# Kernel optimization log

Hardware: AMD Instinct MI355X
Metric: run time of the kernel (lower is better)

## Reference

```python
import jax, jax.numpy as jnp
import numpy as np

B, N = 8, 4096
NPOINT, RADIUS, NSAMPLE = 1024, 0.5, 32
IN_C = 64
MLP = [64, 64, 128]
EPS = 1e-5


def _gather(p, idx):
    # p: (B,N,C), idx: (B,...) int -> (B,...,C)
    return jax.vmap(lambda a, i: a[i])(p, idx)


def farthest_point_sample(xyz, npoint):
    b, n, _ = xyz.shape
    def step(carry, _):
        distance, farthest = carry
        centroid = _gather(xyz, farthest[:, None])              # (B,1,3)
        d = jnp.sum((xyz - centroid) ** 2, axis=-1)             # (B,N)
        distance = jnp.minimum(distance, d)
        nxt = jnp.argmax(distance, axis=-1).astype(jnp.int32)
        return (distance, nxt), farthest
    init = (jnp.full((b, n), 1e10, xyz.dtype), jnp.zeros((b,), jnp.int32))
    _, idx = jax.lax.scan(step, init, None, length=npoint)
    return idx.T                                                 # (B,npoint)


def query_ball_point(radius, nsample, xyz, new_xyz):
    b, n, _ = xyz.shape
    s = new_xyz.shape[1]
    sqr = jnp.sum((new_xyz[:, :, None, :] - xyz[:, None, :, :]) ** 2, axis=-1)  # (B,S,N)
    grp = jnp.broadcast_to(jnp.arange(n, dtype=jnp.int32), (b, s, n))
    grp = jnp.where(sqr > radius ** 2, n, grp)
    grp = jnp.sort(grp, axis=-1)[:, :, :nsample]                 # (B,S,K)
    first = grp[:, :, :1]
    return jnp.where(grp == n, first, grp)


def _sa_forward(xyz, points, params):
    fps_idx = farthest_point_sample(xyz, NPOINT)
    new_xyz = _gather(xyz, fps_idx)                              # (B,S,3)
    idx = query_ball_point(RADIUS, NSAMPLE, xyz, new_xyz)        # (B,S,K)
    grouped_xyz = _gather(xyz, idx)                              # (B,S,K,3)
    grouped_norm = grouped_xyz - new_xyz[:, :, None, :]
    grouped_pts = _gather(points, idx)                           # (B,S,K,C)
    feat = jnp.concatenate([grouped_xyz, grouped_norm, grouped_pts], axis=-1)
    for w, bias, gamma, beta in params:
        feat = jnp.einsum('bski,oi->bsko', feat, w) + bias       # 1x1 conv
        mean = feat.mean(axis=(0, 1, 2))                         # BN (train stats)
        var = feat.var(axis=(0, 1, 2))
        feat = (feat - mean) * jax.lax.rsqrt(var + EPS) * gamma + beta
        feat = jax.nn.relu(feat)
    new_points = feat.max(axis=2)                                # max over neighbors
    return new_xyz, new_points


def setup_inputs() -> dict:
    key = jax.random.key(0)
    ks = jax.random.split(key, 8)
    inp = {
        'xyz': jax.random.normal(ks[0], (B, N, 3), jnp.float32),
        'points': jax.random.normal(ks[1], (B, N, IN_C), jnp.float32),
    }
    last = IN_C + 6
    for li, out in enumerate(MLP):
        inp[f'w{li}'] = jax.random.normal(ks[2 + li], (out, last), jnp.float32) * 0.05
        inp[f'b{li}'] = jnp.zeros((out,), jnp.float32)
        inp[f'g{li}'] = jnp.ones((out,), jnp.float32)
        inp[f'be{li}'] = jnp.zeros((out,), jnp.float32)
        last = out
    return inp


def reference(xyz, points, w0, b0, g0, be0, w1, b1, g1, be1, w2, b2, g2, be2):
    params = [(w0, b0, g0, be0), (w1, b1, g1, be1), (w2, b2, g2, be2)]
    return _sa_forward(xyz, points, params)
```

## Files before the change

kernel.cpp:

```cpp
#include <hip/hip_runtime.h>

#define DI __device__ __forceinline__

#define B_ 8
#define N_ 4096
#define S_ 1024
#define K_ 32
#define M_TOT (B_ * S_ * K_)
#define NBLK 2048
#define NW 4096

typedef short bf16x8 __attribute__((ext_vector_type(8)));
typedef float f32x4 __attribute__((ext_vector_type(4)));

DI float sqdist_rn(float ax, float ay, float az, float bx, float by, float bz) {
    float dx = __fsub_rn(ax, bx);
    float dy = __fsub_rn(ay, by);
    float dz = __fsub_rn(az, bz);
    return __fadd_rn(__fadd_rn(__fmul_rn(dx, dx), __fmul_rn(dy, dy)), __fmul_rn(dz, dz));
}

DI unsigned short f2b(float f) {
    unsigned u = __float_as_uint(f);
    return (unsigned short)((u + 0x7FFFu + ((u >> 16) & 1u)) >> 16);
}
DI float b2f(unsigned short h) { return __uint_as_float(((unsigned)h) << 16); }

template <int CTRL>
DI unsigned long long dpp_u64(unsigned long long v) {
    unsigned lo = (unsigned)__builtin_amdgcn_update_dpp(
        0, (int)(unsigned)v, CTRL, 0xF, 0xF, true);
    unsigned hi = (unsigned)__builtin_amdgcn_update_dpp(
        0, (int)(unsigned)(v >> 32), CTRL, 0xF, 0xF, true);
    return ((unsigned long long)hi << 32) | lo;
}
DI unsigned long long umax64(unsigned long long a, unsigned long long b) {
    return a > b ? a : b;
}

__global__ __launch_bounds__(512) void fps_kernel(const float* __restrict__ xyz,
                                                  float* __restrict__ new_xyz) {
    const int b = blockIdx.x;
    const int t = threadIdx.x;
    const float* X = xyz + (size_t)b * (N_ * 3);
    __shared__ float4 pts[N_];
    __shared__ __align__(16) unsigned long long part[2][8];
    float px[8], py[8], pz[8], dd[8];
#pragma unroll
    for (int j = 0; j < 8; ++j) {
        int p = t + 512 * j;
        float x = X[p * 3 + 0], y = X[p * 3 + 1], z = X[p * 3 + 2];
        px[j] = x; py[j] = y; pz[j] = z; dd[j] = 1e10f;
        pts[p] = make_float4(x, y, z, 0.0f);
    }
    if (t == 0) {
        new_xyz[(size_t)b * (S_ * 3) + 0] = px[0];
        new_xyz[(size_t)b * (S_ * 3) + 1] = py[0];
        new_xyz[(size_t)b * (S_ * 3) + 2] = pz[0];
    }
    __syncthreads();
    float4 cent = pts[0];
    for (int i = 1; i < S_; ++i) {
        unsigned long long k0[8];
#pragma unroll
        for (int j = 0; j < 8; ++j) {
            float d = sqdist_rn(px[j], py[j], pz[j], cent.x, cent.y, cent.z);
            dd[j] = fminf(dd[j], d);
            k0[j] = ((unsigned long long)__float_as_uint(dd[j]) << 32) |
                    (unsigned long long)(~(unsigned)(t + 512 * j));
        }
        k0[0] = umax64(k0[0], k0[1]);
        k0[2] = umax64(k0[2], k0[3]);
        k0[4] = umax64(k0[4], k0[5]);
        k0[6] = umax64(k0[6], k0[7]);
        k0[0] = umax64(k0[0], k0[2]);
        k0[4] = umax64(k0[4], k0[6]);
        unsigned long long key = umax64(k0[0], k0[4]);
        key = umax64(key, dpp_u64<0x111>(key));
        key = umax64(key, dpp_u64<0x112>(key));
        key = umax64(key, dpp_u64<0x114>(key));
        key = umax64(key, dpp_u64<0x118>(key));
        key = umax64(key, dpp_u64<0x142>(key));
        key = umax64(key, dpp_u64<0x143>(key));
        if ((t & 63) == 63) part[i & 1][t >> 6] = key;
        __syncthreads();
        ulonglong2 q0 = *(const ulonglong2*)&part[i & 1][0];
        ulonglong2 q1 = *(const ulonglong2*)&part[i & 1][2];
        ulonglong2 q2 = *(const ulonglong2*)&part[i & 1][4];
        ulonglong2 q3 = *(const ulonglong2*)&part[i & 1][6];
        unsigned long long ka = umax64(umax64(q0.x, q0.y), umax64(q1.x, q1.y));
        unsigned long long kb = umax64(umax64(q2.x, q2.y), umax64(q3.x, q3.y));
        unsigned long long k = umax64(ka, kb);
        unsigned gidx = ~(unsigned)(k & 0xFFFFFFFFull);
        cent = pts[gidx];
        if (t == 0) {
            size_t o3 = ((size_t)b * S_ + i) * 3;
            new_xyz[o3 + 0] = cent.x;
            new_xyz[o3 + 1] = cent.y;
            new_xyz[o3 + 2] = cent.z;
        }
    }
}

__global__ __launch_bounds__(256) void qb_kernel(const float* __restrict__ xyz,
                                                 const float* __restrict__ new_xyz,
                                                 int* __restrict__ idxbuf) {
    const int c = blockIdx.x * 4 + (threadIdx.x >> 6);
    const int lane = threadIdx.x & 63;
    const int b = c >> 10;
    const float* X = xyz + (size_t)b * (N_ * 3);
    const float cx = new_xyz[c * 3 + 0];
    const float cy = new_xyz[c * 3 + 1];
    const float cz = new_xyz[c * 3 + 2];
    int* out = idxbuf + (size_t)c * K_;
    int taken = 0, first = -1;
    for (int ch = 0; ch < 64; ++ch) {
        int p = ch * 64 + lane;
        float d = sqdist_rn(X[p * 3 + 0], X[p * 3 + 1], X[p * 3 + 2], cx, cy, cz);
        bool ok = (d <= 0.25f);
        unsigned long long m = __ballot(ok);
        if (first < 0 && m) first = ch * 64 + (__ffsll((unsigned long long)m) - 1);
        int pos = taken + (int)__popcll(m & ((1ull << lane) - 1ull));
        if (ok && pos < K_) out[pos] = p;
        taken += (int)__popcll(m);
        if (taken >= K_) break;
    }
    int filled = taken < K_ ? taken : K_;
    if (lane >= filled && lane < K_) out[lane] = first;
}

template <int FS, int SLOTS, int CC>
DI void gemm_tile(const float* __restrict__ feat, const float* __restrict__ wl,
                  const float* __restrict__ bias, unsigned short* __restrict__ yout,
                  float* __restrict__ ps, float* __restrict__ pq,
                  int r0, int tid, int blk) {
    const int tr = tid & 15;
    const int tc = tid >> 4;
    float acc[8][CC];
#pragma unroll
    for (int rr = 0; rr < 8; ++rr)
#pragma unroll
        for (int cc = 0; cc < CC; ++cc) acc[rr][cc] = 0.0f;

#pragma unroll 2
    for (int sl = 0; sl < SLOTS; ++sl) {
        float4 xv[8], wv[CC];
#pragma unroll
        for (int rr = 0; rr < 8; ++rr)
            xv[rr] = *(const float4*)&feat[(tr + 16 * rr) * FS + 4 * sl];
#pragma unroll
        for (int cc = 0; cc < CC; ++cc)
            wv[cc] = *(const float4*)&wl[(tc + 16 * cc) * FS + 4 * sl];
#pragma unroll
        for (int rr = 0; rr < 8; ++rr)
#pragma unroll
            for (int cc = 0; cc < CC; ++cc)
                acc[rr][cc] = fmaf(xv[rr].x, wv[cc].x,
                               fmaf(xv[rr].y, wv[cc].y,
                                fmaf(xv[rr].z, wv[cc].z,
                                 fmaf(xv[rr].w, wv[cc].w, acc[rr][cc]))));
    }
    float s1[CC], s2[CC];
#pragma unroll
    for (int cc = 0; cc < CC; ++cc) {
        const int och = tc + 16 * cc;
        const float bv = bias[och];
        s1[cc] = 0.0f; s2[cc] = 0.0f;
#pragma unroll
        for (int rr = 0; rr < 8; ++rr) {
            float y = acc[rr][cc] + bv;
            const int gr = r0 + tr + 16 * rr;
            yout[(size_t)gr * (16 * CC) + och] = f2b(y);
            s1[cc] += y;
            s2[cc] = fmaf(y, y, s2[cc]);
        }
    }
#pragma unroll
    for (int m = 1; m < 16; m <<= 1) {
#pragma unroll
        for (int cc = 0; cc < CC; ++cc) {
            s1[cc] += __shfl_xor(s1[cc], m);
            s2[cc] += __shfl_xor(s2[cc], m);
        }
    }
    if ((tid & 15) == 0) {
#pragma unroll
        for (int cc = 0; cc < CC; ++cc) {
            const int och = tc + 16 * cc;
            ps[och * NBLK + blk] = s1[cc];
            pq[och * NBLK + blk] = s2[cc];
        }
    }
}

__global__ __launch_bounds__(256) void layer1_kernel(
    const float* __restrict__ xyz, const float* __restrict__ points,
    const float* __restrict__ new_xyz, const int* __restrict__ idxbuf,
    const float* __restrict__ W, const float* __restrict__ bias,
    unsigned short* __restrict__ yout, float* __restrict__ ps, float* __restrict__ pq) {
    const int tid = threadIdx.x;
    const int blk = blockIdx.x;
    const int r0 = blk * 128;
    __shared__ float feat[128 * 76];
    __shared__ float wl[64 * 76];
    for (int jj = tid; jj < 64 * 70; jj += 256) {
        int o = jj / 70;
        int i = jj - o * 70;
        int mch = (i < 6) ? i : (i + 2);
        wl[o * 76 + mch] = W[jj];
    }
    if (tid < 128) wl[(tid >> 1) * 76 + 6 + (tid & 1)] = 0.0f;
    {
        const int row = tid >> 1, h = tid & 1;
        const int gr = r0 + row;
        const int b = gr >> 15;
        const int s = (gr >> 5) & 1023;
        const int pi = idxbuf[gr];
        const float* P = points + ((size_t)b * N_ + pi) * 64 + h * 32;
        float* fr = &feat[row * 76];
#pragma unroll
        for (int q = 0; q < 8; ++q) {
            float4 v = *(const float4*)(P + 4 * q);
            *(float4*)(fr + 8 + h * 32 + 4 * q) = v;
        }
        if (h == 0) {
            size_t pb = ((size_t)b * N_ + pi) * 3;
            float x = xyz[pb + 0], y = xyz[pb + 1], z = xyz[pb + 2];
            const float* C = new_xyz + ((size_t)b * S_ + s) * 3;
            fr[0] = x; fr[1] = y; fr[2] = z;
            fr[3] = x - C[0]; fr[4] = y - C[1]; fr[5] = z - C[2];
            fr[6] = 0.0f; fr[7] = 0.0f;
        }
    }
    __syncthreads();
    gemm_tile<76, 18, 4>(feat, wl, bias, yout, ps, pq, r0, tid, blk);
}

template <int OC, bool LAST>
__global__ __launch_bounds__(256) void layerM_kernel(
    const unsigned short* __restrict__ yin,
    const float* __restrict__ scale, const float* __restrict__ shift,
    const float* __restrict__ W, const float* __restrict__ bias,
    unsigned short* __restrict__ yout,
    float* __restrict__ ps, float* __restrict__ pq,
    float* __restrict__ maxb, float* __restrict__ minb) {
    const int tid = threadIdx.x;
    const int blk = blockIdx.x;
    const int r0 = blk * 256;
    __shared__ unsigned short featA[256 * 64];
    __shared__ unsigned short wlT[OC * 64];
    __shared__ float ssc[64], ssh[64];
    if (tid < 64) { ssc[tid] = scale[tid]; ssh[tid] = shift[tid]; }
#pragma unroll
    for (int it = 0; it < OC / 16; ++it) {
        int q = it * 256 + tid;
        int och = q >> 4;
        int qq = q & 15;
        float4 wv = *(const float4*)&W[q * 4];
        uint2 pk;
        pk.x = (unsigned)f2b(wv.x) | ((unsigned)f2b(wv.y) << 16);
        pk.y = (unsigned)f2b(wv.z) | ((unsigned)f2b(wv.w) << 16);
        int idx = och * 64 + (((qq * 8) ^ ((och & 7) << 4)) >> 1);
        *(uint2*)&wlT[idx] = pk;
    }
    __syncthreads();
#pragma unroll
    for (int it = 0; it < 8; ++it) {
        int f = it * 256 + tid;
        int row = f >> 3, g = f & 7;
        uint4 u = *(const uint4*)&yin[(size_t)(r0 + row) * 64 + g * 8];
        int c = g * 8;
        float f0 = fmaxf(fmaf(__uint_as_float(u.x << 16),         ssc[c + 0], ssh[c + 0]), 0.f);
        float f1 = fmaxf(fmaf(__uint_as_float(u.x & 0xFFFF0000u), ssc[c + 1], ssh[c + 1]), 0.f);
        float f2 = fmaxf(fmaf(__uint_as_float(u.y << 16),         ssc[c + 2], ssh[c + 2]), 0.f);
        float f3 = fmaxf(fmaf(__uint_as_float(u.y & 0xFFFF0000u), ssc[c + 3], ssh[c + 3]), 0.f);
        float f4 = fmaxf(fmaf(__uint_as_float(u.z << 16),         ssc[c + 4], ssh[c + 4]), 0.f);
        float f5 = fmaxf(fmaf(__uint_as_float(u.z & 0xFFFF0000u), ssc[c + 5], ssh[c + 5]), 0.f);
        float f6 = fmaxf(fmaf(__uint_as_float(u.w << 16),         ssc[c + 6], ssh[c + 6]), 0.f);
        float f7 = fmaxf(fmaf(__uint_as_float(u.w & 0xFFFF0000u), ssc[c + 7], ssh[c + 7]), 0.f);
        uint4 pk;
        pk.x = (unsigned)f2b(f0) | ((unsigned)f2b(f1) << 16);
        pk.y = (unsigned)f2b(f2) | ((unsigned)f2b(f3) << 16);
        pk.z = (unsigned)f2b(f4) | ((unsigned)f2b(f5) << 16);
        pk.w = (unsigned)f2b(f6) | ((unsigned)f2b(f7) << 16);
        int idx = row * 64 + (((g * 16) ^ ((row & 7) << 4)) >> 1);
        *(uint4*)&featA[idx] = pk;
    }
    __syncthreads();
    const int w = tid >> 6, l = tid & 63;
    const int lr = l & 15, lg = l >> 4;
    const int wrow0 = w * 64;
    f32x4 acc[4][OC / 16];
#pragma unroll
    for (int mf = 0; mf < 4; ++mf)
#pragma unroll
        for (int nf = 0; nf < OC / 16; ++nf)
#pragma unroll
            for (int r = 0; r < 4; ++r) acc[mf][nf][r] = 0.0f;
#pragma unroll
    for (int kc = 0; kc < 2; ++kc) {
        const int kb = kc * 64 + lg * 16;
        bf16x8 bfr[OC / 16];
#pragma unroll
        for (int nf = 0; nf < OC / 16; ++nf) {
            int och = nf * 16 + lr;
            bfr[nf] = *(const bf16x8*)&wlT[och * 64 + ((kb ^ ((och & 7) << 4)) >> 1)];
        }
#pragma unroll
        for (int mf = 0; mf < 4; ++mf) {
            int row = wrow0 + mf * 16 + lr;
            bf16x8 af = *(const bf16x8*)&featA[row * 64 + ((kb ^ ((row & 7) << 4)) >> 1)];
#pragma unroll
            for (int nf = 0; nf < OC / 16; ++nf)
                acc[mf][nf] = __builtin_amdgcn_mfma_f32_16x16x32_bf16(
                    af, bfr[nf], acc[mf][nf], 0, 0, 0);
        }
    }
    const int gwave = blk * 4 + w;
#pragma unroll
    for (int nf = 0; nf < OC / 16; ++nf) {
        const int och = nf * 16 + lr;
        const float bv = bias[och];
        float s1 = 0.f, s2 = 0.f;
        float mx0 = -1e30f, mn0 = 1e30f, mx1 = -1e30f, mn1 = 1e30f;
#pragma unroll
        for (int mf = 0; mf < 4; ++mf) {
#pragma unroll
            for (int r = 0; r < 4; ++r) {
                float y = acc[mf][nf][r] + bv;
                s1 += y;
                s2 = fmaf(y, y, s2);
                if (LAST) {
                    if (mf < 2) { mx0 = fmaxf(mx0, y); mn0 = fminf(mn0, y); }
                    else        { mx1 = fmaxf(mx1, y); mn1 = fminf(mn1, y); }
                } else {
                    int gr = r0 + wrow0 + mf * 16 + lg * 4 + r;
                    yout[(size_t)gr * OC + och] = f2b(y);
                }
            }
        }
        s1 += __shfl_xor(s1, 16); s1 += __shfl_xor(s1, 32);
        s2 += __shfl_xor(s2, 16); s2 += __shfl_xor(s2, 32);
        if (LAST) {
            mx0 = fmaxf(mx0, __shfl_xor(mx0, 16)); mx0 = fmaxf(mx0, __shfl_xor(mx0, 32));
            mn0 = fminf(mn0, __shfl_xor(mn0, 16)); mn0 = fminf(mn0, __shfl_xor(mn0, 32));
            mx1 = fmaxf(mx1, __shfl_xor(mx1, 16)); mx1 = fmaxf(mx1, __shfl_xor(mx1, 32));
            mn1 = fminf(mn1, __shfl_xor(mn1, 16)); mn1 = fminf(mn1, __shfl_xor(mn1, 32));
        }
        if (l < 16) {
            ps[och * NW + gwave] = s1;
            pq[och * NW + gwave] = s2;
            if (LAST) {
                int grp0 = blk * 8 + w * 2;
                maxb[(size_t)grp0 * OC + och] = mx0;
                minb[(size_t)grp0 * OC + och] = mn0;
                maxb[(size_t)(grp0 + 1) * OC + och] = mx1;
                minb[(size_t)(grp0 + 1) * OC + och] = mn1;
            }
        }
    }
}

template <int NPART>
__global__ __launch_bounds__(256) void bn_reduce_kernel(
    const float* __restrict__ ps, const float* __restrict__ pq,
    const float* __restrict__ gamma, const float* __restrict__ beta,
    float* __restrict__ scale, float* __restrict__ shift) {
    const int o = blockIdx.x, t = threadIdx.x;
    float s1 = 0.f, s2 = 0.f;
    for (int i = t; i < NPART; i += 256) {
        s1 += ps[o * NPART + i];
        s2 += pq[o * NPART + i];
    }
#pragma unroll
    for (int m = 32; m >= 1; m >>= 1) { s1 += __shfl_xor(s1, m); s2 += __shfl_xor(s2, m); }
    __shared__ float a1[4], a2[4];
    if ((t & 63) == 0) { a1[t >> 6] = s1; a2[t >> 6] = s2; }
    __syncthreads();
    if (t == 0) {
        float S1 = a1[0] + a1[1] + a1[2] + a1[3];
        float S2 = a2[0] + a2[1] + a2[2] + a2[3];
        const float inv = 1.0f / (float)M_TOT;
        float mean = S1 * inv;
        float var = S2 * inv - mean * mean;
        if (var < 0.f) var = 0.f;
        float rstd = 1.0f / sqrtf(var + 1e-5f);
        float sc = rstd * gamma[o];
        scale[o] = sc;
        shift[o] = beta[o] - mean * sc;
    }
}

__global__ __launch_bounds__(256) void pool2_kernel(
    const float* __restrict__ maxb, const float* __restrict__ minb,
    const float* __restrict__ scale, const float* __restrict__ shift,
    float* __restrict__ outp) {
    int idx = blockIdx.x * 256 + threadIdx.x;
    int och = idx & 127;
    float sc = scale[och], sh = shift[och];
    float a = fmaf(maxb[idx], sc, sh);
    float b = fmaf(minb[idx], sc, sh);
    outp[idx] = fmaxf(fmaxf(a, b), 0.0f);
}

extern "C" void kernel_launch(void* const* d_in, const int* in_sizes, int n_in,
                              void* d_out, int out_size, void* d_ws, size_t ws_size,
                              hipStream_t stream) {
    const float* xyz    = (const float*)d_in[0];
    const float* points = (const float*)d_in[1];
    const float* w0  = (const float*)d_in[2];
    const float* b0  = (const float*)d_in[3];
    const float* g0  = (const float*)d_in[4];
    const float* be0 = (const float*)d_in[5];
    const float* w1  = (const float*)d_in[6];
    const float* b1  = (const float*)d_in[7];
    const float* g1  = (const float*)d_in[8];
    const float* be1 = (const float*)d_in[9];
    const float* w2  = (const float*)d_in[10];
    const float* b2  = (const float*)d_in[11];
    const float* g2  = (const float*)d_in[12];
    const float* be2 = (const float*)d_in[13];

    float* out = (float*)d_out;
    char* ws = (char*)d_ws;
    int*   idxbuf = (int*)ws;
    float* ps  = (float*)(ws + (1 << 20));
    float* pq  = (float*)(ws + (3 << 20));
    float* st  = (float*)(ws + (5 << 20));
    float *sc0 = st,        *sh0 = st + 128;
    float *sc1 = st + 256,  *sh1 = st + 384;
    float *sc2 = st + 512,  *sh2 = st + 640;
    float* maxb = (float*)(ws + (6 << 20));
    float* minb = (float*)(ws + (10 << 20));
    unsigned short* y1 = (unsigned short*)(ws + (14 << 20));
    unsigned short* y2 = (unsigned short*)(ws + (46 << 20));

    fps_kernel<<<8, 512, 0, stream>>>(xyz, out);
    qb_kernel<<<2048, 256, 0, stream>>>(xyz, out, idxbuf);
    layer1_kernel<<<NBLK, 256, 0, stream>>>(xyz, points, out, idxbuf, w0, b0, y1, ps, pq);
    bn_reduce_kernel<NBLK><<<64, 256, 0, stream>>>(ps, pq, g0, be0, sc0, sh0);
    layerM_kernel<64, false><<<M_TOT / 256, 256, 0, stream>>>(
        y1, sc0, sh0, w1, b1, y2, ps, pq, nullptr, nullptr);
    bn_reduce_kernel<NW><<<64, 256, 0, stream>>>(ps, pq, g1, be1, sc1, sh1);
    layerM_kernel<128, true><<<M_TOT / 256, 256, 0, stream>>>(
        y2, sc1, sh1, w2, b2, nullptr, ps, pq, maxb, minb);
    bn_reduce_kernel<NW><<<128, 256, 0, stream>>>(ps, pq, g2, be2, sc2, sh2);
    pool2_kernel<<<4096, 256, 0, stream>>>(maxb, minb, sc2, sh2, out + 24576);
}
```

Baseline: 853.3 us.

## Fuse FPS, ball query and layer1 into a persistent cooperative mega-kernel

Merges the farthest-point-sampling, ball-query and first MLP layer kernels into one cooperative persistent kernel. Eight blocks run FPS and publish progress counters every 32 centroids with release atomics. The remaining blocks poll those counters, then run the ball query and layer-1 GEMM on finished centroids. This overlaps the serial FPS latency with downstream work and drops the idx buffer round-trip. The cost is spin-wait polling, a larger union shared-memory footprint, and a dependence on all blocks being co-resident.

```diff
diff --git a/kernel.cpp b/kernel.cpp
--- a/kernel.cpp
+++ b/kernel.cpp
@@ -38,20 +38,22 @@
     return a > b ? a : b;
 }
 
-__global__ __launch_bounds__(512) void fps_kernel(const float* __restrict__ xyz,
-                                                  float* __restrict__ new_xyz) {
+struct FpsSh { float4 pts[N_]; unsigned long long part[2][8]; };
+struct WrkSh { float feat[128 * 76]; float wl[64 * 76]; int idxl[128]; };
+union MegaSh { FpsSh f; WrkSh w; };
+
+DI void fps_role(const float* __restrict__ xyz, float* __restrict__ new_xyz,
+                 unsigned* __restrict__ cnt, MegaSh& sh) {
     const int b = blockIdx.x;
     const int t = threadIdx.x;
     const float* X = xyz + (size_t)b * (N_ * 3);
-    __shared__ float4 pts[N_];
-    __shared__ __align__(16) unsigned long long part[2][8];
     float px[8], py[8], pz[8], dd[8];
 #pragma unroll
     for (int j = 0; j < 8; ++j) {
         int p = t + 512 * j;
         float x = X[p * 3 + 0], y = X[p * 3 + 1], z = X[p * 3 + 2];
         px[j] = x; py[j] = y; pz[j] = z; dd[j] = 1e10f;
-        pts[p] = make_float4(x, y, z, 0.0f);
+        sh.f.pts[p] = make_float4(x, y, z, 0.0f);
     }
     if (t == 0) {
         new_xyz[(size_t)b * (S_ * 3) + 0] = px[0];
@@ -59,7 +61,7 @@
         new_xyz[(size_t)b * (S_ * 3) + 2] = pz[0];
     }
     __syncthreads();
-    float4 cent = pts[0];
+    float4 cent = sh.f.pts[0];
     for (int i = 1; i < S_; ++i) {
         unsigned long long k0[8];
 #pragma unroll
@@ -82,158 +84,165 @@
         key = umax64(key, dpp_u64<0x118>(key));
         key = umax64(key, dpp_u64<0x142>(key));
         key = umax64(key, dpp_u64<0x143>(key));
-        if ((t & 63) == 63) part[i & 1][t >> 6] = key;
+        if ((t & 63) == 63) sh.f.part[i & 1][t >> 6] = key;
         __syncthreads();
-        ulonglong2 q0 = *(const ulonglong2*)&part[i & 1][0];
-        ulonglong2 q1 = *(const ulonglong2*)&part[i & 1][2];
-        ulonglong2 q2 = *(const ulonglong2*)&part[i & 1][4];
-        ulonglong2 q3 = *(const ulonglong2*)&part[i & 1][6];
+        ulonglong2 q0 = *(const ulonglong2*)&sh.f.part[i & 1][0];
+        ulonglong2 q1 = *(const ulonglong2*)&sh.f.part[i & 1][2];
+        ulonglong2 q2 = *(const ulonglong2*)&sh.f.part[i & 1][4];
+        ulonglong2 q3 = *(const ulonglong2*)&sh.f.part[i & 1][6];
         unsigned long long ka = umax64(umax64(q0.x, q0.y), umax64(q1.x, q1.y));
         unsigned long long kb = umax64(umax64(q2.x, q2.y), umax64(q3.x, q3.y));
         unsigned long long k = umax64(ka, kb);
         unsigned gidx = ~(unsigned)(k & 0xFFFFFFFFull);
-        cent = pts[gidx];
+        cent = sh.f.pts[gidx];
         if (t == 0) {
             size_t o3 = ((size_t)b * S_ + i) * 3;
             new_xyz[o3 + 0] = cent.x;
             new_xyz[o3 + 1] = cent.y;
             new_xyz[o3 + 2] = cent.z;
-        }
-    }
-}
-
-__global__ __launch_bounds__(256) void qb_kernel(const float* __restrict__ xyz,
-                                                 const float* __restrict__ new_xyz,
-                                                 int* __restrict__ idxbuf) {
-    const int c = blockIdx.x * 4 + (threadIdx.x >> 6);
-    const int lane = threadIdx.x & 63;
-    const int b = c >> 10;
-    const float* X = xyz + (size_t)b * (N_ * 3);
-    const float cx = new_xyz[c * 3 + 0];
-    const float cy = new_xyz[c * 3 + 1];
-    const float cz = new_xyz[c * 3 + 2];
-    int* out = idxbuf + (size_t)c * K_;
-    int taken = 0, first = -1;
-    for (int ch = 0; ch < 64; ++ch) {
-        int p = ch * 64 + lane;
-        float d = sqdist_rn(X[p * 3 + 0], X[p * 3 + 1], X[p * 3 + 2], cx, cy, cz);
-        bool ok = (d <= 0.25f);
-        unsigned long long m = __ballot(ok);
-        if (first < 0 && m) first = ch * 64 + (__ffsll((unsigned long long)m) - 1);
-        int pos = taken + (int)__popcll(m & ((1ull << lane) - 1ull));
-        if (ok && pos < K_) out[pos] = p;
-        taken += (int)__popcll(m);
-        if (taken >= K_) break;
-    }
-    int filled = taken < K_ ? taken : K_;
-    if (lane >= filled && lane < K_) out[lane] = first;
-}
-
-template <int FS, int SLOTS, int CC>
-DI void gemm_tile(const float* __restrict__ feat, const float* __restrict__ wl,
-                  const float* __restrict__ bias, unsigned short* __restrict__ yout,
-                  float* __restrict__ ps, float* __restrict__ pq,
-                  int r0, int tid, int blk) {
+            if ((i & 31) == 31) {
+                __threadfence();
+                __hip_atomic_store(&cnt[b], (unsigned)(i + 1),
+                                   __ATOMIC_RELEASE, __HIP_MEMORY_SCOPE_AGENT);
+            }
+        }
+    }
+}
+
+DI void gemm512(const float* __restrict__ feat, const float* __restrict__ wl,
+                const float* __restrict__ bias, unsigned short* __restrict__ yout,
+                float* __restrict__ ps, float* __restrict__ pq, int tile, int tid) {
     const int tr = tid & 15;
     const int tc = tid >> 4;
-    float acc[8][CC];
-#pragma unroll
-    for (int rr = 0; rr < 8; ++rr)
-#pragma unroll
-        for (int cc = 0; cc < CC; ++cc) acc[rr][cc] = 0.0f;
-
+    const int r0 = tile * 128;
+    float acc[8][2];
+#pragma unroll
+    for (int rr = 0; rr < 8; ++rr) { acc[rr][0] = 0.f; acc[rr][1] = 0.f; }
 #pragma unroll 2
-    for (int sl = 0; sl < SLOTS; ++sl) {
-        float4 xv[8], wv[CC];
+    for (int sl = 0; sl < 18; ++sl) {
+        float4 xv[8], wv[2];
 #pragma unroll
         for (int rr = 0; rr < 8; ++rr)
-            xv[rr] = *(const float4*)&feat[(tr + 16 * rr) * FS + 4 * sl];
-#pragma unroll
-        for (int cc = 0; cc < CC; ++cc)
-            wv[cc] = *(const float4*)&wl[(tc + 16 * cc) * FS + 4 * sl];
+            xv[rr] = *(const float4*)&feat[(tr + 16 * rr) * 76 + 4 * sl];
+#pragma unroll
+        for (int cc = 0; cc < 2; ++cc)
+            wv[cc] = *(const float4*)&wl[(tc + 32 * cc) * 76 + 4 * sl];
 #pragma unroll
         for (int rr = 0; rr < 8; ++rr)
 #pragma unroll
-            for (int cc = 0; cc < CC; ++cc)
+            for (int cc = 0; cc < 2; ++cc)
                 acc[rr][cc] = fmaf(xv[rr].x, wv[cc].x,
                                fmaf(xv[rr].y, wv[cc].y,
                                 fmaf(xv[rr].z, wv[cc].z,
                                  fmaf(xv[rr].w, wv[cc].w, acc[rr][cc]))));
     }
-    float s1[CC], s2[CC];
-#pragma unroll
-    for (int cc = 0; cc < CC; ++cc) {
-        const int och = tc + 16 * cc;
+#pragma unroll
+    for (int cc = 0; cc < 2; ++cc) {
+        const int och = tc + 32 * cc;
         const float bv = bias[och];
-        s1[cc] = 0.0f; s2[cc] = 0.0f;
+        float s1 = 0.f, s2 = 0.f;
 #pragma unroll
         for (int rr = 0; rr < 8; ++rr) {
             float y = acc[rr][cc] + bv;
-            const int gr = r0 + tr + 16 * rr;
-            yout[(size_t)gr * (16 * CC) + och] = f2b(y);
-            s1[cc] += y;
-            s2[cc] = fmaf(y, y, s2[cc]);
-        }
-    }
-#pragma unroll
-    for (int m = 1; m < 16; m <<= 1) {
-#pragma unroll
-        for (int cc = 0; cc < CC; ++cc) {
-            s1[cc] += __shfl_xor(s1[cc], m);
-            s2[cc] += __shfl_xor(s2[cc], m);
-        }
-    }
-    if ((tid & 15) == 0) {
-#pragma unroll
-        for (int cc = 0; cc < CC; ++cc) {
-            const int och = tc + 16 * cc;
-            ps[och * NBLK + blk] = s1[cc];
-            pq[och * NBLK + blk] = s2[cc];
-        }
-    }
-}
-
-__global__ __launch_bounds__(256) void layer1_kernel(
+            yout[(size_t)(r0 + tr + 16 * rr) * 64 + och] = f2b(y);
+            s1 += y;
+            s2 = fmaf(y, y, s2);
+        }
+#pragma unroll
+        for (int m = 1; m < 16; m <<= 1) {
+            s1 += __shfl_xor(s1, m);
+            s2 += __shfl_xor(s2, m);
+        }
+        if ((tid & 15) == 0) {
+            ps[och * NBLK + tile] = s1;
+            pq[och * NBLK + tile] = s2;
+        }
+    }
+}
+
+DI void worker_role(const float* __restrict__ xyz, const float* __restrict__ points,
+                    const float* __restrict__ new_xyz, const float* __restrict__ W0,
+                    const float* __restrict__ bias0, unsigned short* __restrict__ yout,
+                    float* __restrict__ ps, float* __restrict__ pq,
+                    const unsigned* __restrict__ cnt, MegaSh& sh, int nWrk) {
+    const int t = threadIdx.x;
+    for (int g = (int)blockIdx.x - 8; g < 2048; g += nWrk) {
+        const int q = g >> 3;
+        const int b = g & 7;
+        const int s0 = q * 4;
+        const int tile = b * 256 + q;
+        if (t == 0) {
+            while (__hip_atomic_load(&cnt[b], __ATOMIC_ACQUIRE,
+                                     __HIP_MEMORY_SCOPE_AGENT) < (unsigned)(s0 + 4))
+                __builtin_amdgcn_s_sleep(32);
+        }
+        __syncthreads();
+        const int w = t >> 6, lane = t & 63;
+        if (w < 4) {
+            const int c = b * 1024 + s0 + w;
+            const float* X = xyz + (size_t)b * (N_ * 3);
+            const float cx = new_xyz[c * 3 + 0];
+            const float cy = new_xyz[c * 3 + 1];
+            const float cz = new_xyz[c * 3 + 2];
+            int* out = &sh.w.idxl[w * K_];
+            int taken = 0, first = -1;
+            for (int ch = 0; ch < 64; ++ch) {
+                int p = ch * 64 + lane;
+                float d = sqdist_rn(X[p * 3 + 0], X[p * 3 + 1], X[p * 3 + 2], cx, cy, cz);
+                bool ok = (d <= 0.25f);
+                unsigned long long m = __ballot(ok);
+                if (first < 0 && m) first = ch * 64 + (__ffsll((unsigned long long)m) - 1);
+                int pos = taken + (int)__popcll(m & ((1ull << lane) - 1ull));
+                if (ok && pos < K_) out[pos] = p;
+                taken += (int)__popcll(m);
+                if (taken >= K_) break;
+            }
+            int filled = taken < K_ ? taken : K_;
+            if (lane >= filled && lane < K_) out[lane] = first;
+        }
+        __syncthreads();
+        for (int jj = t; jj < 64 * 70; jj += 512) {
+            int o = jj / 70;
+            int i2 = jj - o * 70;
+            int mch = (i2 < 6) ? i2 : (i2 + 2);
+            sh.w.wl[o * 76 + mch] = W0[jj];
+        }
+        if (t < 128) sh.w.wl[(t >> 1) * 76 + 6 + (t & 1)] = 0.0f;
+        {
+            const int row = t >> 2, h = t & 3;
+            const int k = row & 31, cloc = row >> 5;
+            const int pi = sh.w.idxl[cloc * 32 + k];
+            const float* P = points + ((size_t)b * N_ + pi) * 64 + h * 16;
+            float* fr = &sh.w.feat[row * 76];
+#pragma unroll
+            for (int qq = 0; qq < 4; ++qq)
+                *(float4*)(fr + 8 + h * 16 + 4 * qq) = *(const float4*)(P + 4 * qq);
+            if (h == 0) {
+                size_t pb = ((size_t)b * N_ + pi) * 3;
+                float x = xyz[pb + 0], y = xyz[pb + 1], z = xyz[pb + 2];
+                const float* C = new_xyz + ((size_t)b * S_ + s0 + cloc) * 3;
+                fr[0] = x; fr[1] = y; fr[2] = z;
+                fr[3] = x - C[0]; fr[4] = y - C[1]; fr[5] = z - C[2];
+                fr[6] = 0.0f; fr[7] = 0.0f;
+            }
+        }
+        __syncthreads();
+        gemm512(sh.w.feat, sh.w.wl, bias0, yout, ps, pq, tile, t);
+        __syncthreads();
+    }
+}
+
+__global__ __launch_bounds__(512) void mega_kernel(
     const float* __restrict__ xyz, const float* __restrict__ points,
-    const float* __restrict__ new_xyz, const int* __restrict__ idxbuf,
-    const float* __restrict__ W, const float* __restrict__ bias,
-    unsigned short* __restrict__ yout, float* __restrict__ ps, float* __restrict__ pq) {
-    const int tid = threadIdx.x;
-    const int blk = blockIdx.x;
-    const int r0 = blk * 128;
-    __shared__ float feat[128 * 76];
-    __shared__ float wl[64 * 76];
-    for (int jj = tid; jj < 64 * 70; jj += 256) {
-        int o = jj / 70;
-        int i = jj - o * 70;
-        int mch = (i < 6) ? i : (i + 2);
-        wl[o * 76 + mch] = W[jj];
-    }
-    if (tid < 128) wl[(tid >> 1) * 76 + 6 + (tid & 1)] = 0.0f;
-    {
-        const int row = tid >> 1, h = tid & 1;
-        const int gr = r0 + row;
-        const int b = gr >> 15;
-        const int s = (gr >> 5) & 1023;
-        const int pi = idxbuf[gr];
-        const float* P = points + ((size_t)b * N_ + pi) * 64 + h * 32;
-        float* fr = &feat[row * 76];
-#pragma unroll
-        for (int q = 0; q < 8; ++q) {
-            float4 v = *(const float4*)(P + 4 * q);
-            *(float4*)(fr + 8 + h * 32 + 4 * q) = v;
-        }
-        if (h == 0) {
-            size_t pb = ((size_t)b * N_ + pi) * 3;
-            float x = xyz[pb + 0], y = xyz[pb + 1], z = xyz[pb + 2];
-            const float* C = new_xyz + ((size_t)b * S_ + s) * 3;
-            fr[0] = x; fr[1] = y; fr[2] = z;
-            fr[3] = x - C[0]; fr[4] = y - C[1]; fr[5] = z - C[2];
-            fr[6] = 0.0f; fr[7] = 0.0f;
-        }
-    }
-    __syncthreads();
-    gemm_tile<76, 18, 4>(feat, wl, bias, yout, ps, pq, r0, tid, blk);
+    float* __restrict__ new_xyz, const float* __restrict__ w0,
+    const float* __restrict__ b0, unsigned short* __restrict__ y1,
+    float* __restrict__ ps, float* __restrict__ pq,
+    unsigned* __restrict__ cnt, int nWrk) {
+    __shared__ MegaSh sh;
+    if (blockIdx.x < 8)
+        fps_role(xyz, new_xyz, cnt, sh);
+    else
+        worker_role(xyz, points, new_xyz, w0, b0, y1, ps, pq, cnt, sh, nWrk);
 }
 
 template <int OC, bool LAST>
@@ -423,7 +432,7 @@
 
     float* out = (float*)d_out;
     char* ws = (char*)d_ws;
-    int*   idxbuf = (int*)ws;
+    unsigned* cnt = (unsigned*)ws;
     float* ps  = (float*)(ws + (1 << 20));
     float* pq  = (float*)(ws + (3 << 20));
     float* st  = (float*)(ws + (5 << 20));
@@ -435,9 +444,19 @@
     unsigned short* y1 = (unsigned short*)(ws + (14 << 20));
     unsigned short* y2 = (unsigned short*)(ws + (46 << 20));
 
-    fps_kernel<<<8, 512, 0, stream>>>(xyz, out);
-    qb_kernel<<<2048, 256, 0, stream>>>(xyz, out, idxbuf);
-    layer1_kernel<<<NBLK, 256, 0, stream>>>(xyz, points, out, idxbuf, w0, b0, y1, ps, pq);
+    int blocksPerCU = 0;
+    hipOccupancyMaxActiveBlocksPerMultiprocessor(&blocksPerCU, mega_kernel, 512, 0);
+    if (blocksPerCU < 1) blocksPerCU = 1;
+    int grid = blocksPerCU * 256;
+    if (grid > 2056) grid = 2056;
+    int nWrk = grid - 8;
+
+    hipMemsetAsync(cnt, 0, 8 * sizeof(unsigned), stream);
+
+    void* args[] = {(void*)&xyz, (void*)&points, (void*)&out, (void*)&w0, (void*)&b0,
+                    (void*)&y1, (void*)&ps, (void*)&pq, (void*)&cnt, (void*)&nWrk};
+    hipLaunchCooperativeKernel(mega_kernel, dim3(grid), dim3(512), args, 0, stream);
+
     bn_reduce_kernel<NBLK><<<64, 256, 0, stream>>>(ps, pq, g0, be0, sc0, sh0);
     layerM_kernel<64, false><<<M_TOT / 256, 256, 0, stream>>>(
         y1, sc0, sh0, w1, b1, y2, ps, pq, nullptr, nullptr);
```

Result: no change. 849.0 us (-0.5%).
